# Kernel tuning notes

Measured on AMD Instinct MI355X. Metric: run time of the kernel, lower is better.

The kernel has to match this reference:

```python
import jax, jax.numpy as jnp
import numpy as np

EMBED = 1024  # point_net_embedding_dim
H1, H2 = 512, 256  # head_hidden_layer_sizes


def _init(key, shape, fan_in):
    return jax.random.normal(key, shape, dtype=jnp.float32) / jnp.sqrt(jnp.float32(fan_in))


def setup_inputs() -> dict:
    key = jax.random.key(0)
    ks = jax.random.split(key, 13)
    B, N = 256, 1024
    x = jax.random.normal(ks[0], (B, N, 3), dtype=jnp.float32)
    # PointNet shared per-point MLP: 3 -> 64 -> 128 -> EMBED (ReLU), max-pool over points
    W1 = _init(ks[1], (3, 64), 3);        b1 = jnp.zeros((64,), jnp.float32)
    W2 = _init(ks[2], (64, 128), 64);     b2 = jnp.zeros((128,), jnp.float32)
    W3 = _init(ks[3], (128, EMBED), 128); b3 = jnp.zeros((EMBED,), jnp.float32)
    # Head MLP: EMBED -> 512 -> 256 -> 9 (no final activation)
    Wh1 = _init(ks[4], (EMBED, H1), EMBED); bh1 = jnp.zeros((H1,), jnp.float32)
    Wh2 = _init(ks[5], (H1, H2), H1);       bh2 = jnp.zeros((H2,), jnp.float32)
    Wh3 = _init(ks[6], (H2, 9), H2);        bh3 = jnp.zeros((9,), jnp.float32)
    return {"x": x, "W1": W1, "b1": b1, "W2": W2, "b2": b2, "W3": W3, "b3": b3,
            "Wh1": Wh1, "bh1": bh1, "Wh2": Wh2, "bh2": bh2, "Wh3": Wh3, "bh3": bh3}


def svd_projection(M):
    # Project raw 3x3 matrices onto SO(3): R = U diag(1,1,det(U V^T)) V^T
    U, S, Vh = jnp.linalg.svd(M, full_matrices=False)
    det = jnp.linalg.det(jnp.einsum('...ij,...jk->...ik', U, Vh))
    d = jnp.stack([jnp.ones_like(det), jnp.ones_like(det), det], axis=-1)  # [..., 3]
    return jnp.einsum('...ij,...j,...jk->...ik', U, d, Vh)


def reference(x, W1, b1, W2, b2, W3, b3, Wh1, bh1, Wh2, bh2, Wh3, bh3):
    # Shared per-point MLP (ReLU), final_activation=ReLU, then max-pool over points
    h = jax.nn.relu(x @ W1 + b1)          # [B, N, 64]
    h = jax.nn.relu(h @ W2 + b2)          # [B, N, 128]
    h = jax.nn.relu(h @ W3 + b3)          # [B, N, EMBED]
    g = jnp.max(h, axis=-2)               # [B, EMBED] global feature
    # Head MLP -> raw 3x3
    z = jax.nn.relu(g @ Wh1 + bh1)
    z = jax.nn.relu(z @ Wh2 + bh2)
    raw = (z @ Wh3 + bh3).reshape(*x.shape[:-2], 3, 3)
    return svd_projection(raw)
```

## Files before the change

kernel.cpp:

```cpp
#include <hip/hip_runtime.h>
#include <math.h>

typedef _Float16 f16;
typedef _Float16 f16x8 __attribute__((ext_vector_type(8)));
typedef float f32x4 __attribute__((ext_vector_type(4)));


__global__ __launch_bounds__(256, 2) void pointnet_l12(
    const float* __restrict__ x,
    const float* __restrict__ W1, const float* __restrict__ b1,
    const float* __restrict__ W2, const float* __restrict__ b2,
    f16* __restrict__ h2)
{
    __shared__ float xs[512*3];
    __shared__ float w1s[192], b1s[64], b2s[128];
    __shared__ __align__(16) f16 h2s[128*136];

    int tid = threadIdx.x;
    int P0 = blockIdx.x * 512;
    for (int i = tid; i < 1536; i += 256) xs[i] = x[(size_t)P0*3 + i];
    if (tid < 192) w1s[tid] = W1[tid];
    else b1s[tid - 192] = b1[tid - 192];
    if (tid < 128) b2s[tid] = b2[tid];

    int lane = tid & 63, wid = tid >> 6;
    int wr = wid & 1, wc = wid >> 1;
    int lrow = lane & 15, quad = lane >> 4;

    f16x8 bf[4][2];
#pragma unroll
    for (int ct = 0; ct < 4; ct++)
#pragma unroll
        for (int kc = 0; kc < 2; kc++) {
            int col = wc*64 + ct*16 + lrow;
#pragma unroll
            for (int j = 0; j < 8; j++)
                bf[ct][kc][j] = (f16)W2[(size_t)(kc*32 + quad*8 + j)*128 + col];
        }

    __syncthreads();

    for (int mt = 0; mt < 4; mt++) {
        f32x4 acc[4][4];
#pragma unroll
        for (int rt = 0; rt < 4; rt++)
#pragma unroll
            for (int ct = 0; ct < 4; ct++)
                acc[rt][ct] = (f32x4){0.f, 0.f, 0.f, 0.f};

#pragma unroll
        for (int kc = 0; kc < 2; kc++) {
            float wa[8], wb[8], wcv[8], bv[8];
#pragma unroll
            for (int j = 0; j < 8; j++) {
                int k = kc*32 + quad*8 + j;
                wa[j] = w1s[k]; wb[j] = w1s[64+k]; wcv[j] = w1s[128+k]; bv[j] = b1s[k];
            }
            f16x8 af[4];
#pragma unroll
            for (int rt = 0; rt < 4; rt++) {
                int p = mt*128 + wr*64 + rt*16 + lrow;
                float x0 = xs[p*3], x1 = xs[p*3+1], x2 = xs[p*3+2];
#pragma unroll
                for (int j = 0; j < 8; j++) {
                    float v = fmaf(x2, wcv[j], fmaf(x1, wb[j], fmaf(x0, wa[j], bv[j])));
                    af[rt][j] = (f16)fmaxf(v, 0.f);
                }
            }
#pragma unroll
            for (int rt = 0; rt < 4; rt++)
#pragma unroll
                for (int ct = 0; ct < 4; ct++)
                    acc[rt][ct] = __builtin_amdgcn_mfma_f32_16x16x32_f16(af[rt], bf[ct][kc], acc[rt][ct], 0, 0, 0);
        }

        __syncthreads();
#pragma unroll
        for (int rt = 0; rt < 4; rt++)
#pragma unroll
            for (int ct = 0; ct < 4; ct++) {
                int col  = wc*64 + ct*16 + lrow;
                float bb = b2s[col];
                int rowb = wr*64 + rt*16 + quad*4;
#pragma unroll
                for (int r = 0; r < 4; r++) {
                    float v = fmaxf(acc[rt][ct][r] + bb, 0.f);
                    h2s[(rowb + r)*136 + col] = (f16)v;
                }
            }
        __syncthreads();
        size_t gch = (((size_t)P0 + (size_t)mt*128) >> 4) * 256;
#pragma unroll
        for (int i = 0; i < 8; i++) {
            int o = i*256 + tid;
            int gg = o >> 8, rem = o & 255;
            int kc = rem >> 6, qd = (rem >> 4) & 3, lr = rem & 15;
            int row = gg*16 + lr, c = kc*4 + qd;
            f16x8 v = *(const f16x8*)(h2s + row*136 + c*8);
            *(f16x8*)(h2 + (gch + o)*8) = v;
        }
    }
}

__global__ __launch_bounds__(256, 2) void pointnet_l3_max(
    const f16* __restrict__ h2,
    const float* __restrict__ W3,
    const float* __restrict__ b3,
    float* __restrict__ g)
{
    int i  = blockIdx.x;
    int b  = i & 255, nb = i >> 8;
    int tid = threadIdx.x;
    int lane = tid & 63, wid = tid >> 6;
    int lrow = lane & 15, quad = lane >> 4;
    int col0 = nb*256 + wid*64;

    f16x8 bf[4][4];
#pragma unroll
    for (int ct = 0; ct < 4; ct++)
#pragma unroll
        for (int kc = 0; kc < 4; kc++) {
            int col = col0 + ct*16 + lrow;
#pragma unroll
            for (int j = 0; j < 8; j++)
                bf[ct][kc][j] = (f16)W3[(size_t)(kc*32 + quad*8 + j)*1024 + col];
        }

    float cmax[4] = {-3.0e38f, -3.0e38f, -3.0e38f, -3.0e38f};
    const f16* abase = h2 + (size_t)b * 131072 + lane*8;

    for (int m0 = 0; m0 < 1024; m0 += 128) {
        int gbase = m0 >> 4;
#pragma unroll
        for (int half = 0; half < 2; half++) {
            f32x4 acc[4][4];
#pragma unroll
            for (int rt = 0; rt < 4; rt++)
#pragma unroll
                for (int ct = 0; ct < 4; ct++)
                    acc[rt][ct] = (f32x4){0.f, 0.f, 0.f, 0.f};
#pragma unroll
            for (int kc = 0; kc < 4; kc++) {
                f16x8 af[4];
#pragma unroll
                for (int rt = 0; rt < 4; rt++)
                    af[rt] = *(const f16x8*)(abase + (size_t)(gbase + half*4 + rt)*2048 + kc*512);
#pragma unroll
                for (int rt = 0; rt < 4; rt++)
#pragma unroll
                    for (int ct = 0; ct < 4; ct++)
                        acc[rt][ct] = __builtin_amdgcn_mfma_f32_16x16x32_f16(af[rt], bf[ct][kc], acc[rt][ct], 0, 0, 0);
            }
#pragma unroll
            for (int rt = 0; rt < 4; rt++)
#pragma unroll
                for (int ct = 0; ct < 4; ct++)
#pragma unroll
                    for (int r = 0; r < 4; r += 2)
                        cmax[ct] = fmaxf(fmaxf(acc[rt][ct][r], acc[rt][ct][r+1]), cmax[ct]);
        }
    }

#pragma unroll
    for (int ct = 0; ct < 4; ct++) {
        cmax[ct] = fmaxf(cmax[ct], __shfl_xor(cmax[ct], 16, 64));
        cmax[ct] = fmaxf(cmax[ct], __shfl_xor(cmax[ct], 32, 64));
    }
    if (quad == 0) {
#pragma unroll
        for (int ct = 0; ct < 4; ct++) {
            int cg = col0 + ct*16 + lrow;
            g[(size_t)b*1024 + cg] = fmaxf(cmax[ct] + b3[cg], 0.f);
        }
    }
}

__global__ __launch_bounds__(256) void head_l1(
    const float* __restrict__ g, const float* __restrict__ Wh1,
    float* __restrict__ zp1)
{
    __shared__ float gs4[4][256];
    int cb = blockIdx.x, bb = blockIdx.y, kc = blockIdx.z;
    int tid = threadIdx.x;
    int b0 = bb * 4;
    int kbase = kc * 256;
#pragma unroll
    for (int j = 0; j < 4; j++) {
        int i = tid + j*256;
        gs4[i >> 8][i & 255] = g[(size_t)(b0 + (i >> 8))*1024 + kbase + (i & 255)];
    }
    __syncthreads();

    int c = cb*256 + tid;
    float acc[4] = {0.f, 0.f, 0.f, 0.f};
#pragma unroll 1
    for (int k = 0; k < 256; k += 8) {
        float w[8];
#pragma unroll
        for (int j = 0; j < 8; j++) w[j] = Wh1[(size_t)(kbase+k+j)*512 + c];
#pragma unroll
        for (int r = 0; r < 4; r++) {
            float4 a = *(const float4*)&gs4[r][k];
            float4 bq = *(const float4*)&gs4[r][k+4];
            acc[r] = fmaf(a.x, w[0], acc[r]);
            acc[r] = fmaf(a.y, w[1], acc[r]);
            acc[r] = fmaf(a.z, w[2], acc[r]);
            acc[r] = fmaf(a.w, w[3], acc[r]);
            acc[r] = fmaf(bq.x, w[4], acc[r]);
            acc[r] = fmaf(bq.y, w[5], acc[r]);
            acc[r] = fmaf(bq.z, w[6], acc[r]);
            acc[r] = fmaf(bq.w, w[7], acc[r]);
        }
    }
#pragma unroll
    for (int r = 0; r < 4; r++)
        zp1[((size_t)kc*256 + b0 + r)*512 + c] = acc[r];
}

__global__ __launch_bounds__(256) void head_l2(
    const float* __restrict__ zp1, const float* __restrict__ bh1,
    const float* __restrict__ Wh2, float* __restrict__ zp2)
{
    __shared__ float z1s[2][128];
    int bb = blockIdx.x, kc2 = blockIdx.y;
    int tid = threadIdx.x;
    int b0 = bb * 2;
    int kb = kc2 * 128;
    {
        int row = tid >> 7, kk = tid & 127;
        int col = kb + kk;
        float v = bh1[col];
#pragma unroll
        for (int j = 0; j < 4; j++)
            v += zp1[((size_t)j*256 + b0 + row)*512 + col];
        z1s[row][kk] = fmaxf(v, 0.f);
    }
    __syncthreads();

    int c = tid;
    float acc0 = 0.f, acc1 = 0.f;
#pragma unroll 1
    for (int k = 0; k < 128; k += 8) {
        float w[8];
#pragma unroll
        for (int j = 0; j < 8; j++) w[j] = Wh2[(size_t)(kb+k+j)*256 + c];
        float4 a0 = *(const float4*)&z1s[0][k];
        float4 a1 = *(const float4*)&z1s[0][k+4];
        float4 d0 = *(const float4*)&z1s[1][k];
        float4 d1 = *(const float4*)&z1s[1][k+4];
        acc0 = fmaf(a0.x, w[0], acc0);  acc1 = fmaf(d0.x, w[0], acc1);
        acc0 = fmaf(a0.y, w[1], acc0);  acc1 = fmaf(d0.y, w[1], acc1);
        acc0 = fmaf(a0.z, w[2], acc0);  acc1 = fmaf(d0.z, w[2], acc1);
        acc0 = fmaf(a0.w, w[3], acc0);  acc1 = fmaf(d0.w, w[3], acc1);
        acc0 = fmaf(a1.x, w[4], acc0);  acc1 = fmaf(d1.x, w[4], acc1);
        acc0 = fmaf(a1.y, w[5], acc0);  acc1 = fmaf(d1.y, w[5], acc1);
        acc0 = fmaf(a1.z, w[6], acc0);  acc1 = fmaf(d1.z, w[6], acc1);
        acc0 = fmaf(a1.w, w[7], acc0);  acc1 = fmaf(d1.w, w[7], acc1);
    }
    zp2[((size_t)kc2*256 + b0    )*256 + c] = acc0;
    zp2[((size_t)kc2*256 + b0 + 1)*256 + c] = acc1;
}

__device__ inline void jrot(double S[3][3], double V[3][3], int p, int q)
{
    double apq = S[p][q];
    if (fabs(apq) < 1e-36) return;
    double tau = (S[q][q] - S[p][p]) / (2.0 * apq);
    double t = (tau >= 0.0 ? 1.0 : -1.0) / (fabs(tau) + sqrt(1.0 + tau*tau));
    double c = 1.0 / sqrt(1.0 + t*t);
    double s = t * c;
    for (int k = 0; k < 3; k++) {
        double skp = S[k][p], skq = S[k][q];
        S[k][p] = c*skp - s*skq;  S[k][q] = s*skp + c*skq;
    }
    for (int k = 0; k < 3; k++) {
        double spk = S[p][k], sqk = S[q][k];
        S[p][k] = c*spk - s*sqk;  S[q][k] = s*spk + c*sqk;
    }
    for (int k = 0; k < 3; k++) {
        double vkp = V[k][p], vkq = V[k][q];
        V[k][p] = c*vkp - s*vkq;  V[k][q] = s*vkp + c*vkq;
    }
}

__device__ void svd_so3(const float* Mf, float* Rout)
{
    double M[3][3], S[3][3], V[3][3];
    for (int i = 0; i < 3; i++)
        for (int j = 0; j < 3; j++) M[i][j] = (double)Mf[3*i+j];
    for (int i = 0; i < 3; i++)
        for (int j = 0; j < 3; j++)
            S[i][j] = M[0][i]*M[0][j] + M[1][i]*M[1][j] + M[2][i]*M[2][j];
    for (int i = 0; i < 3; i++)
        for (int j = 0; j < 3; j++) V[i][j] = (i == j) ? 1.0 : 0.0;
    for (int it = 0; it < 10; it++) {
        jrot(S, V, 0, 1); jrot(S, V, 0, 2); jrot(S, V, 1, 2);
    }
    double lam[3] = {S[0][0], S[1][1], S[2][2]};
    int i0 = 0, i1 = 1, i2 = 2, tt;
    if (lam[i0] < lam[i1]) { tt = i0; i0 = i1; i1 = tt; }
    if (lam[i0] < lam[i2]) { tt = i0; i0 = i2; i2 = tt; }
    if (lam[i1] < lam[i2]) { tt = i1; i1 = i2; i2 = tt; }
    double v0[3], v1[3], v2[3];
    for (int k = 0; k < 3; k++) { v0[k] = V[k][i0]; v1[k] = V[k][i1]; v2[k] = V[k][i2]; }
    double u1[3], u2[3], u3[3];
    for (int i = 0; i < 3; i++) u1[i] = M[i][0]*v0[0] + M[i][1]*v0[1] + M[i][2]*v0[2];
    double n1 = sqrt(u1[0]*u1[0] + u1[1]*u1[1] + u1[2]*u1[2]) + 1e-300;
    for (int i = 0; i < 3; i++) u1[i] /= n1;
    for (int i = 0; i < 3; i++) u2[i] = M[i][0]*v1[0] + M[i][1]*v1[1] + M[i][2]*v1[2];
    double d12 = u1[0]*u2[0] + u1[1]*u2[1] + u1[2]*u2[2];
    for (int i = 0; i < 3; i++) u2[i] -= d12*u1[i];
    double n2 = sqrt(u2[0]*u2[0] + u2[1]*u2[1] + u2[2]*u2[2]) + 1e-300;
    for (int i = 0; i < 3; i++) u2[i] /= n2;
    u3[0] = u1[1]*u2[2] - u1[2]*u2[1];
    u3[1] = u1[2]*u2[0] - u1[0]*u2[2];
    u3[2] = u1[0]*u2[1] - u1[1]*u2[0];
    double c12x = v1[1]*v2[2] - v1[2]*v2[1];
    double c12y = v1[2]*v2[0] - v1[0]*v2[2];
    double c12z = v1[0]*v2[1] - v1[1]*v2[0];
    double detV = v0[0]*c12x + v0[1]*c12y + v0[2]*c12z;
    for (int i = 0; i < 3; i++)
        for (int j = 0; j < 3; j++)
            Rout[3*i+j] = (float)(u1[i]*v0[j] + u2[i]*v1[j] + detV*u3[i]*v2[j]);
}

__global__ __launch_bounds__(128) void head_l3_svd(
    const float* __restrict__ zp2, const float* __restrict__ bh2,
    const float* __restrict__ Wh3, const float* __restrict__ bh3,
    float* __restrict__ out)
{
    __shared__ float z2s[8][256];
    __shared__ float wh3s[2304];
    __shared__ float raws[8][12];
    int b0 = blockIdx.x * 8;
    int tid = threadIdx.x;

    for (int i = tid; i < 2304; i += 128) wh3s[i] = Wh3[i];
    for (int i = tid; i < 8*256; i += 128) {
        int row = i >> 8, kk = i & 255;
        float v = bh2[kk];
#pragma unroll
        for (int j = 0; j < 4; j++)
            v += zp2[((size_t)j*256 + b0 + row)*256 + kk];
        z2s[row][kk] = fmaxf(v, 0.f);
    }
    __syncthreads();

    if (tid < 72) {
        int r = tid / 9, c = tid % 9;
        float acc = bh3[c];
#pragma unroll 8
        for (int k = 0; k < 256; k++) acc = fmaf(z2s[r][k], wh3s[k*9 + c], acc);
        raws[r][c] = acc;
    }
    __syncthreads();

    if (tid < 8) svd_so3(&raws[tid][0], out + (size_t)(b0 + tid)*9);
}

extern "C" void kernel_launch(void* const* d_in, const int* in_sizes, int n_in,
                              void* d_out, int out_size, void* d_ws, size_t ws_size,
                              hipStream_t stream)
{
    const float* x   = (const float*)d_in[0];
    const float* W1  = (const float*)d_in[1];
    const float* b1  = (const float*)d_in[2];
    const float* W2  = (const float*)d_in[3];
    const float* b2  = (const float*)d_in[4];
    const float* W3  = (const float*)d_in[5];
    const float* b3  = (const float*)d_in[6];
    const float* Wh1 = (const float*)d_in[7];
    const float* bh1 = (const float*)d_in[8];
    const float* Wh2 = (const float*)d_in[9];
    const float* bh2 = (const float*)d_in[10];
    const float* Wh3 = (const float*)d_in[11];
    const float* bh3 = (const float*)d_in[12];
    float* out = (float*)d_out;

    char* ws = (char*)d_ws;
    f16*   h2  = (f16*)ws;
    float* g   = (float*)(ws + (size_t)67108864);
    float* zp1 = (float*)(ws + (size_t)67108864 + 1048576);
    float* zp2 = (float*)(ws + (size_t)67108864 + 1048576 + 2097152);

    pointnet_l12<<<512, 256, 0, stream>>>(x, W1, b1, W2, b2, h2);
    pointnet_l3_max<<<1024, 256, 0, stream>>>(h2, W3, b3, g);
    dim3 gridH1(2, 64, 4);
    head_l1<<<gridH1, 256, 0, stream>>>(g, Wh1, zp1);
    dim3 gridH2(128, 4);
    head_l2<<<gridH2, 256, 0, stream>>>(zp1, bh1, Wh2, zp2);
    head_l3_svd<<<32, 128, 0, stream>>>(zp2, bh2, Wh3, bh3, out);
}
```

Measured before the change: 193.0 us.

## Pre-transpose W3 to fp16 and retile layer-3 max kernel across wave grid

Adds a small kernel that transposes W3 into a k-contiguous fp16 buffer, so each wave loads its B fragments with vector loads instead of strided scalar fp32 loads plus converts. The layer-3 kernel is retiled so waves form a 2x2 grid: each wave covers 128 columns and half the rows, and holds 8x4 B fragments in registers. Partial maxima are merged through shared memory before the bias, ReLU and store. This halves A-fragment reloads per column tile but raises register pressure, adds one extra launch and needs a block barrier.

```diff
diff --git a/kernel.cpp b/kernel.cpp
--- a/kernel.cpp
+++ b/kernel.cpp
@@ -5,6 +5,26 @@
 typedef _Float16 f16x8 __attribute__((ext_vector_type(8)));
 typedef float f32x4 __attribute__((ext_vector_type(4)));
 
+
+__global__ __launch_bounds__(256) void prep_w3t(
+    const float* __restrict__ w3, f16* __restrict__ w3t)
+{
+    __shared__ float t[64][65];
+    int kt = blockIdx.x & 1, nt = blockIdx.x >> 1;
+    int k0 = kt*64, n0 = nt*64;
+    int tid = threadIdx.x;
+#pragma unroll
+    for (int j = 0; j < 16; j++) {
+        int r = j*4 + (tid >> 6), c = tid & 63;
+        t[r][c] = w3[(size_t)(k0+r)*1024 + n0 + c];
+    }
+    __syncthreads();
+#pragma unroll
+    for (int j = 0; j < 16; j++) {
+        int n = j*4 + (tid >> 6), k = tid & 63;
+        w3t[(size_t)(n0+n)*128 + k0 + k] = (f16)t[k][n];
+    }
+}
 
 __global__ __launch_bounds__(256, 2) void pointnet_l12(
     const float* __restrict__ x,
@@ -104,74 +124,74 @@
 
 __global__ __launch_bounds__(256, 2) void pointnet_l3_max(
     const f16* __restrict__ h2,
-    const float* __restrict__ W3,
+    const f16* __restrict__ w3t,
     const float* __restrict__ b3,
     float* __restrict__ g)
 {
+    __shared__ float redbuf[2][256];
+
     int i  = blockIdx.x;
     int b  = i & 255, nb = i >> 8;
     int tid = threadIdx.x;
     int lane = tid & 63, wid = tid >> 6;
+    int wr = wid & 1, wc = wid >> 1;
     int lrow = lane & 15, quad = lane >> 4;
-    int col0 = nb*256 + wid*64;
-
-    f16x8 bf[4][4];
-#pragma unroll
-    for (int ct = 0; ct < 4; ct++)
-#pragma unroll
-        for (int kc = 0; kc < 4; kc++) {
-            int col = col0 + ct*16 + lrow;
-#pragma unroll
-            for (int j = 0; j < 8; j++)
-                bf[ct][kc][j] = (f16)W3[(size_t)(kc*32 + quad*8 + j)*1024 + col];
+    int col0 = nb*256 + wc*128;
+
+    f16x8 bf[8][4];
+#pragma unroll
+    for (int ct = 0; ct < 8; ct++)
+#pragma unroll
+        for (int kc = 0; kc < 4; kc++)
+            bf[ct][kc] = *(const f16x8*)(w3t + (size_t)(col0 + ct*16 + lrow)*128 + kc*32 + quad*8);
+
+    float cmax[8];
+#pragma unroll
+    for (int ct = 0; ct < 8; ct++) cmax[ct] = -3.0e38f;
+
+    const f16* abase = h2 + (size_t)b * 131072 + lane*8;
+
+#pragma unroll 1
+    for (int mt = 0; mt < 8; mt++) {
+#pragma unroll
+        for (int rt = 0; rt < 4; rt++) {
+            int t = mt*8 + wr*4 + rt;
+            f16x8 af[4];
+#pragma unroll
+            for (int kc = 0; kc < 4; kc++)
+                af[kc] = *(const f16x8*)(abase + (size_t)t*2048 + kc*512);
+            f32x4 acc[8];
+#pragma unroll
+            for (int ct = 0; ct < 8; ct++)
+                acc[ct] = (f32x4){0.f, 0.f, 0.f, 0.f};
+#pragma unroll
+            for (int kc = 0; kc < 4; kc++)
+#pragma unroll
+                for (int ct = 0; ct < 8; ct++)
+                    acc[ct] = __builtin_amdgcn_mfma_f32_16x16x32_f16(af[kc], bf[ct][kc], acc[ct], 0, 0, 0);
+#pragma unroll
+            for (int ct = 0; ct < 8; ct++)
+                cmax[ct] = fmaxf(fmaxf(fmaxf(acc[ct][0], acc[ct][1]),
+                                       fmaxf(acc[ct][2], acc[ct][3])), cmax[ct]);
         }
-
-    float cmax[4] = {-3.0e38f, -3.0e38f, -3.0e38f, -3.0e38f};
-    const f16* abase = h2 + (size_t)b * 131072 + lane*8;
-
-    for (int m0 = 0; m0 < 1024; m0 += 128) {
-        int gbase = m0 >> 4;
-#pragma unroll
-        for (int half = 0; half < 2; half++) {
-            f32x4 acc[4][4];
-#pragma unroll
-            for (int rt = 0; rt < 4; rt++)
-#pragma unroll
-                for (int ct = 0; ct < 4; ct++)
-                    acc[rt][ct] = (f32x4){0.f, 0.f, 0.f, 0.f};
-#pragma unroll
-            for (int kc = 0; kc < 4; kc++) {
-                f16x8 af[4];
-#pragma unroll
-                for (int rt = 0; rt < 4; rt++)
-                    af[rt] = *(const f16x8*)(abase + (size_t)(gbase + half*4 + rt)*2048 + kc*512);
-#pragma unroll
-                for (int rt = 0; rt < 4; rt++)
-#pragma unroll
-                    for (int ct = 0; ct < 4; ct++)
-                        acc[rt][ct] = __builtin_amdgcn_mfma_f32_16x16x32_f16(af[rt], bf[ct][kc], acc[rt][ct], 0, 0, 0);
-            }
-#pragma unroll
-            for (int rt = 0; rt < 4; rt++)
-#pragma unroll
-                for (int ct = 0; ct < 4; ct++)
-#pragma unroll
-                    for (int r = 0; r < 4; r += 2)
-                        cmax[ct] = fmaxf(fmaxf(acc[rt][ct][r], acc[rt][ct][r+1]), cmax[ct]);
-        }
-    }
-
-#pragma unroll
-    for (int ct = 0; ct < 4; ct++) {
+    }
+
+#pragma unroll
+    for (int ct = 0; ct < 8; ct++) {
         cmax[ct] = fmaxf(cmax[ct], __shfl_xor(cmax[ct], 16, 64));
         cmax[ct] = fmaxf(cmax[ct], __shfl_xor(cmax[ct], 32, 64));
     }
     if (quad == 0) {
 #pragma unroll
-        for (int ct = 0; ct < 4; ct++) {
-            int cg = col0 + ct*16 + lrow;
-            g[(size_t)b*1024 + cg] = fmaxf(cmax[ct] + b3[cg], 0.f);
-        }
+        for (int ct = 0; ct < 8; ct++)
+            redbuf[wr][wc*128 + ct*16 + lrow] = cmax[ct];
+    }
+    __syncthreads();
+    {
+        int c = tid;
+        float v = fmaxf(redbuf[0][c], redbuf[1][c]);
+        int cg = nb*256 + c;
+        g[(size_t)b*1024 + cg] = fmaxf(v + b3[cg], 0.f);
     }
 }
 
@@ -379,12 +399,14 @@
 
     char* ws = (char*)d_ws;
     f16*   h2  = (f16*)ws;
-    float* g   = (float*)(ws + (size_t)67108864);
-    float* zp1 = (float*)(ws + (size_t)67108864 + 1048576);
-    float* zp2 = (float*)(ws + (size_t)67108864 + 1048576 + 2097152);
-
+    f16*   w3t = (f16*)(ws + (size_t)67108864);
+    float* g   = (float*)(ws + (size_t)67108864 + 262144);
+    float* zp1 = (float*)(ws + (size_t)67108864 + 262144 + 1048576);
+    float* zp2 = (float*)(ws + (size_t)67108864 + 262144 + 1048576 + 2097152);
+
+    prep_w3t<<<32, 256, 0, stream>>>(W3, w3t);
     pointnet_l12<<<512, 256, 0, stream>>>(x, W1, b1, W2, b2, h2);
-    pointnet_l3_max<<<1024, 256, 0, stream>>>(h2, W3, b3, g);
+    pointnet_l3_max<<<1024, 256, 0, stream>>>(h2, w3t, b3, g);
     dim3 gridH1(2, 64, 4);
     head_l1<<<gridH1, 256, 0, stream>>>(g, Wh1, zp1);
     dim3 gridH2(128, 4);
```

Result: no change. 194.2 us (+0.7%).
